# Kernel tuning notes

Hardware: AMD Instinct MI355X
Metric: run time of the kernel (lower is better)

The kernel has to match this reference:

```python
import jax, jax.numpy as jnp
import numpy as np

N = 100000   # nodes
E = 1600000  # edges (avg degree 16)
D = 64       # out_channels (in_channels == out_channels, so no zero-padding step)
L = 2        # GatedGraphConv num_layers


def setup_inputs() -> dict:
    key = jax.random.key(0)
    ks = jax.random.split(key, 11)
    w = lambda k, shape: jax.random.normal(k, shape, jnp.float32) * 0.05
    return {
        "x": jax.random.normal(ks[0], (N, D), jnp.float32),
        "edge_index": jax.random.randint(ks[1], (2, E), 0, N, dtype=jnp.int64),
        "conv_w": w(ks[2], (L, D, D)),        # GatedGraphConv per-layer message weight
        "gru_w_ih": w(ks[3], (3 * D, D)),     # GRUCell input->hidden (r|z|n)
        "gru_w_hh": w(ks[4], (3 * D, D)),     # GRUCell hidden->hidden (r|z|n)
        "gru_b_ih": w(ks[5], (3 * D,)),
        "gru_b_hh": w(ks[6], (3 * D,)),
        "lin_w": w(ks[7], (D, D)),            # nn.Linear(out, out)
        "lin_b": w(ks[8], (D,)),
        "attn_w": w(ks[9], (1, D)),           # nn.Linear(out, 1)
        "attn_b": w(ks[10], (1,)),
    }


def reference(x, edge_index, conv_w, gru_w_ih, gru_w_hh, gru_b_ih, gru_b_hh,
              lin_w, lin_b, attn_w, attn_b):
    src, dst = edge_index[0], edge_index[1]
    h = x  # in_channels == out_channels -> no padding
    for i in range(L):
        m = h @ conv_w[i]  # [N, D] transformed messages
        # gather at source nodes, scatter-add into target nodes
        agg = jax.ops.segment_sum(m[src], dst, num_segments=N)  # [N, D]
        # GRUCell(agg, h)
        gi = agg @ gru_w_ih.T + gru_b_ih  # [N, 3D]
        gh = h @ gru_w_hh.T + gru_b_hh    # [N, 3D]
        i_r, i_z, i_n = jnp.split(gi, 3, axis=1)
        h_r, h_z, h_n = jnp.split(gh, 3, axis=1)
        r = jax.nn.sigmoid(i_r + h_r)
        z = jax.nn.sigmoid(i_z + h_z)
        n = jnp.tanh(i_n + r * h_n)
        h = (1.0 - z) * n + z * h
    y = jax.nn.relu(h) @ lin_w.T + lin_b                 # [N, D]
    attn = jax.nn.softmax(y @ attn_w.T + attn_b, axis=0) # [N, 1], softmax over nodes
    return (attn * y).sum(axis=0, keepdims=True)          # [1, D]
```

## Files before the change

kernel.cpp:

```cpp
#include <hip/hip_runtime.h>


typedef __attribute__((ext_vector_type(8))) short s8v;
typedef __attribute__((ext_vector_type(4))) float f32x4;

#define CSR_CAP 12288

__device__ __forceinline__ unsigned short f32_bf16_rn(float x) {
  unsigned u = __float_as_uint(x);
  u += 0x7FFF + ((u >> 16) & 1);
  return (unsigned short)(u >> 16);
}

__device__ __forceinline__ int wave_incl_scan(int v, int lane) {
#pragma unroll
  for (int d = 1; d < 64; d <<= 1) {
    int u = __shfl_up(v, d);
    if (lane >= d) v += u;
  }
  return v;
}

__device__ __forceinline__ int detect_is64(const int* ei, int E) {
  int nz = 0;
  int lim = (E < 512) ? E : 512;
  for (int i = threadIdx.x; i < lim; i += blockDim.x)
    nz |= (ei[2 * i + 1] != 0);
  return __syncthreads_or(nz) ? 0 : 1;
}

__device__ __forceinline__ void load_edge(const int* ei, int E, int is64,
                                          int e, int& s, int& d) {
  if (is64) { s = ei[2 * e]; d = ei[2 * (E + e)]; }
  else      { s = ei[e];     d = ei[E + e]; }
}

__global__ __launch_bounds__(256) void count_kernel(
    const int* __restrict__ ei, int E,
    int* __restrict__ G, int P, int perBlk, int NB) {
  __shared__ int hist[512];
  int tid = threadIdx.x, b = blockIdx.x;
  for (int i = tid; i < 512; i += 256) hist[i] = 0;
  int is64 = detect_is64(ei, E);
  __syncthreads();
  int e0 = b * perBlk, e1 = min(e0 + perBlk, E);
  for (int e = e0 + tid; e < e1; e += 256) {
    int s, d; load_edge(ei, E, is64, e, s, d);
    atomicAdd(&hist[d >> 8], 1);
  }
  __syncthreads();
  for (int i = tid; i < P; i += 256) G[i * NB + b] = hist[i];
}

__global__ __launch_bounds__(256) void scan2a(int* __restrict__ G,
                                              int* __restrict__ total, int NB) {
  __shared__ int wsum[4];
  int p = blockIdx.x, tid = threadIdx.x, lane = tid & 63, wv = tid >> 6;
  int v = G[p * NB + tid];
  int incl = wave_incl_scan(v, lane);
  if (lane == 63) wsum[wv] = incl;
  __syncthreads();
  if (tid == 0) {
    int a = wsum[0], b2 = wsum[1], c = wsum[2], d = wsum[3];
    total[p] = a + b2 + c + d;
    wsum[0] = 0; wsum[1] = a; wsum[2] = a + b2; wsum[3] = a + b2 + c;
  }
  __syncthreads();
  G[p * NB + tid] = incl - v + wsum[wv];
}

__global__ void scan2b(const int* __restrict__ total, int* __restrict__ partStart,
                       int P) {
  int lane = threadIdx.x;
  int running = 0;
  for (int base = 0; base < P; base += 64) {
    int idx = base + lane;
    int v = (idx < P) ? total[idx] : 0;
    int incl = wave_incl_scan(v, lane);
    int tot = __shfl(incl, 63);
    if (idx < P) partStart[idx] = running + incl - v;
    running += tot;
  }
  if (lane == 0) partStart[P] = running;
}

__global__ __launch_bounds__(256) void scatter_kernel(
    const int* __restrict__ ei, int E,
    const int* __restrict__ G, const int* __restrict__ partStart,
    int* __restrict__ bucket, int P, int perBlk, int NB) {
  __shared__ int cur[512];
  int tid = threadIdx.x, b = blockIdx.x;
  int is64 = detect_is64(ei, E);
  for (int i = tid; i < P; i += 256) cur[i] = partStart[i] + G[i * NB + b];
  __syncthreads();
  int e0 = b * perBlk, e1 = min(e0 + perBlk, E);
  for (int e = e0 + tid; e < e1; e += 256) {
    int s, d; load_edge(ei, E, is64, e, s, d);
    int pos = atomicAdd(&cur[d >> 8], 1);
    bucket[pos] = ((d & 255) << 17) | s;
  }
}

__global__ __launch_bounds__(256) void buildcsr_kernel(
    const int* __restrict__ partStart, const int* __restrict__ bucket,
    int* __restrict__ row_ptr, int* __restrict__ col, int N) {
  __shared__ int stage[CSR_CAP];
  __shared__ int hist[256];
  __shared__ int cur[256];
  __shared__ int wsum[4];
  int p = blockIdx.x, tid = threadIdx.x;
  int beg = partStart[p], end = partStart[p + 1];
  int cnt = end - beg;
  int base = p << 8;
  hist[tid] = 0;
  __syncthreads();
  bool staged = (cnt <= CSR_CAP);
  if (staged) {
    for (int i = tid; i < cnt; i += 256) {
      int v = bucket[beg + i];
      stage[i] = v;
      atomicAdd(&hist[(v >> 17) & 255], 1);
    }
  } else {
    for (int i = tid; i < cnt; i += 256)
      atomicAdd(&hist[(bucket[beg + i] >> 17) & 255], 1);
  }
  __syncthreads();
  int lane = tid & 63, wv = tid >> 6;
  int v = hist[tid];
  int incl = wave_incl_scan(v, lane);
  if (lane == 63) wsum[wv] = incl;
  __syncthreads();
  if (tid == 0) {
    int s0 = wsum[0], s1 = wsum[1], s2 = wsum[2];
    wsum[0] = 0; wsum[1] = s0; wsum[2] = s0 + s1; wsum[3] = s0 + s1 + s2;
  }
  __syncthreads();
  int excl = incl - v + wsum[wv];
  cur[tid] = beg + excl;
  if (base + tid < N) {
    if (tid == 0) row_ptr[base] = beg;
    row_ptr[base + tid + 1] = beg + excl + v;
  }
  __syncthreads();
  if (staged) {
    for (int i = tid; i < cnt; i += 256) {
      int v2 = stage[i];
      int pos = atomicAdd(&cur[(v2 >> 17) & 255], 1);
      col[pos] = v2 & 0x1FFFF;
    }
  } else {
    for (int i = tid; i < cnt; i += 256) {
      int v2 = bucket[beg + i];
      int pos = atomicAdd(&cur[(v2 >> 17) & 255], 1);
      col[pos] = v2 & 0x1FFFF;
    }
  }
}

__global__ void wprep_kernel(const float* __restrict__ conv_w,
                             const float* __restrict__ w_ih,
                             const float* __restrict__ whh,
                             const float* __restrict__ lin_w,
                             unsigned short* __restrict__ Bt,
                             unsigned short* __restrict__ Lt) {
  int idx = blockIdx.x * blockDim.x + threadIdx.x;
  if (idx < 65536) {
    int l = idx >> 15;
    int rr = idx & 32767;
    int c = rr >> 7, p = rr & 127;
    int g = c >> 6, ch = c & 63;
    float val = 0.f;
    if (p < 64) {
      int j = (g == 0) ? ch : (g == 1) ? 64 + ch : (g == 2) ? 128 + ch : -1;
      if (j >= 0) {
        const float* C = conv_w + l * 4096 + p * 64;
        const float* W = w_ih + j * 64;
#pragma unroll 8
        for (int k = 0; k < 64; k++) val += C[k] * W[k];
      }
    } else {
      int q = p - 64;
      if (g == 0)      val = whh[ch * 64 + q];
      else if (g == 1) val = whh[(64 + ch) * 64 + q];
      else if (g == 3) val = whh[(128 + ch) * 64 + q];
    }
    unsigned short hi = f32_bf16_rn(val);
    float fh = __uint_as_float((unsigned)hi << 16);
    unsigned short lo = f32_bf16_rn(val - fh);
    size_t base = (size_t)l * 65536;
    Bt[base + (size_t)c * 128 + p] = hi;
    Bt[base + 32768 + (size_t)c * 128 + p] = lo;
  } else if (idx < 65536 + 4096) {
    int i2 = idx - 65536;
    float val = lin_w[i2];
    unsigned short hi = f32_bf16_rn(val);
    float fh = __uint_as_float((unsigned)hi << 16);
    unsigned short lo = f32_bf16_rn(val - fh);
    Lt[i2] = hi;
    Lt[4096 + i2] = lo;
  }
}

__global__ __launch_bounds__(256) void cvt16_kernel(
    const float* __restrict__ in, unsigned short* __restrict__ out, int n8) {
  int idx = blockIdx.x * blockDim.x + threadIdx.x;
  if (idx >= n8) return;
  const float4* p = (const float4*)(in + (size_t)idx * 8);
  float4 v0 = p[0], v1 = p[1];
  uint4 o;
  o.x = (unsigned)f32_bf16_rn(v0.x) | ((unsigned)f32_bf16_rn(v0.y) << 16);
  o.y = (unsigned)f32_bf16_rn(v0.z) | ((unsigned)f32_bf16_rn(v0.w) << 16);
  o.z = (unsigned)f32_bf16_rn(v1.x) | ((unsigned)f32_bf16_rn(v1.y) << 16);
  o.w = (unsigned)f32_bf16_rn(v1.z) | ((unsigned)f32_bf16_rn(v1.w) << 16);
  *(uint4*)(out + (size_t)idx * 8) = o;
}

__global__ __launch_bounds__(256) void gather_kernel(
    const unsigned short* __restrict__ hb, const int* __restrict__ row_ptr,
    const int* __restrict__ col, float* __restrict__ sout, int N) {
  int gt = blockIdx.x * blockDim.x + threadIdx.x;
  int n = gt >> 6, lane = gt & 63;
  if (n >= N) return;
  int grp = lane >> 4, q = lane & 15;
  int beg = row_ptr[n], end = row_ptr[n + 1];
  float4 a0 = make_float4(0.f, 0.f, 0.f, 0.f);
  float4 a1 = make_float4(0.f, 0.f, 0.f, 0.f);
  int e = beg + grp;
  for (; e + 4 < end; e += 8) {
    int s0 = col[e], s1 = col[e + 4];
    uint2 r0 = *(const uint2*)(hb + (size_t)s0 * 64 + q * 4);
    uint2 r1 = *(const uint2*)(hb + (size_t)s1 * 64 + q * 4);
    a0.x += __uint_as_float(r0.x << 16);
    a0.y += __uint_as_float(r0.x & 0xFFFF0000u);
    a0.z += __uint_as_float(r0.y << 16);
    a0.w += __uint_as_float(r0.y & 0xFFFF0000u);
    a1.x += __uint_as_float(r1.x << 16);
    a1.y += __uint_as_float(r1.x & 0xFFFF0000u);
    a1.z += __uint_as_float(r1.y << 16);
    a1.w += __uint_as_float(r1.y & 0xFFFF0000u);
  }
  if (e < end) {
    int s0 = col[e];
    uint2 r0 = *(const uint2*)(hb + (size_t)s0 * 64 + q * 4);
    a0.x += __uint_as_float(r0.x << 16);
    a0.y += __uint_as_float(r0.x & 0xFFFF0000u);
    a0.z += __uint_as_float(r0.y << 16);
    a0.w += __uint_as_float(r0.y & 0xFFFF0000u);
  }
  a0.x += a1.x; a0.y += a1.y; a0.z += a1.z; a0.w += a1.w;
#pragma unroll
  for (int off = 16; off <= 32; off <<= 1) {
    a0.x += __shfl_xor(a0.x, off);
    a0.y += __shfl_xor(a0.y, off);
    a0.z += __shfl_xor(a0.z, off);
    a0.w += __shfl_xor(a0.w, off);
  }
  if (grp == 0) *(float4*)(sout + (size_t)n * 64 + q * 4) = a0;
}

__global__ __launch_bounds__(256, 2) void gemm_gru_kernel(
    const float* __restrict__ sb, const float* __restrict__ hin,
    float* __restrict__ hout, unsigned short* __restrict__ hb16,
    const unsigned short* __restrict__ bt,
    const float* __restrict__ b_ih, const float* __restrict__ b_hh,
    int N, int ntiles, int wb16) {
  __shared__ short Alds[2 * 64 * 136];
  const int tid = threadIdx.x;
  const int lane = tid & 63, w = tid >> 6;
  const int l15 = lane & 15, ko = (lane >> 4) * 8;

  s8v Bh[4][4], Bl[4][4];
  {
    const int col = 16 * w + l15;
#pragma unroll
    for (int c = 0; c < 4; c++)
#pragma unroll
      for (int kk = 0; kk < 4; kk++) {
        size_t o = (size_t)(64 * c + col) * 128 + kk * 32 + ko;
        Bh[c][kk] = *(const s8v*)(bt + o);
        Bl[c][kk] = *(const s8v*)(bt + 32768 + o);
      }
  }
  const int ch = 16 * w + l15;
  const float br = b_ih[ch] + b_hh[ch];
  const float bz = b_ih[64 + ch] + b_hh[64 + ch];
  const float bin_ = b_ih[128 + ch];
  const float bhn = b_hh[128 + ch];
  const int q4 = (lane >> 4) * 4;
  const int sr = tid >> 2, part = tid & 3;

  for (int tile = blockIdx.x; tile < ntiles; tile += gridDim.x) {
    const int nb = tile * 64;
    {
      int node = nb + sr;
      f32x4 v[8];
      if (node < N) {
        const float* base = (part < 2) ? (sb + (size_t)node * 64 + part * 32)
                                       : (hin + (size_t)node * 64 + (part - 2) * 32);
#pragma unroll
        for (int i = 0; i < 8; i++) v[i] = *(const f32x4*)(base + 4 * i);
      } else {
#pragma unroll
        for (int i = 0; i < 8; i++) v[i] = (f32x4)(0.f);
      }
      short* ah = &Alds[sr * 136 + part * 32];
#pragma unroll
      for (int i2 = 0; i2 < 4; i2++) {
        s8v hv, lv;
#pragma unroll
        for (int e = 0; e < 8; e++) {
          float x = v[i2 * 2 + (e >> 2)][e & 3];
          unsigned short hb = f32_bf16_rn(x);
          float fh = __uint_as_float((unsigned)hb << 16);
          unsigned short lb = f32_bf16_rn(x - fh);
          hv[e] = (short)hb;
          lv[e] = (short)lb;
        }
        *(s8v*)(ah + i2 * 8) = hv;
        *(s8v*)(ah + 64 * 136 + i2 * 8) = lv;
      }
    }
    __syncthreads();

    f32x4 acc[4][4];
#pragma unroll
    for (int m = 0; m < 4; m++)
#pragma unroll
      for (int c = 0; c < 4; c++) acc[m][c] = (f32x4)(0.f);

#pragma unroll
    for (int m = 0; m < 4; m++) {
      const short* arow = &Alds[(16 * m + l15) * 136 + ko];
#pragma unroll
      for (int kk = 0; kk < 4; kk++) {
        s8v a_h = *(const s8v*)(arow + kk * 32);
        s8v a_l = *(const s8v*)(arow + 64 * 136 + kk * 32);
#pragma unroll
        for (int c = 0; c < 4; c++) {
          acc[m][c] = __builtin_amdgcn_mfma_f32_16x16x32_bf16(a_h, Bh[c][kk], acc[m][c], 0, 0, 0);
          acc[m][c] = __builtin_amdgcn_mfma_f32_16x16x32_bf16(a_h, Bl[c][kk], acc[m][c], 0, 0, 0);
          acc[m][c] = __builtin_amdgcn_mfma_f32_16x16x32_bf16(a_l, Bh[c][kk], acc[m][c], 0, 0, 0);
        }
      }
    }

#pragma unroll
    for (int m = 0; m < 4; m++) {
#pragma unroll
      for (int g = 0; g < 4; g++) {
        int loc = 16 * m + q4 + g;
        int node = nb + loc;
        if (node < N) {
          unsigned hi = (unsigned short)Alds[loc * 136 + 64 + ch];
          unsigned lo = (unsigned short)Alds[64 * 136 + loc * 136 + 64 + ch];
          float hold = __uint_as_float(hi << 16) + __uint_as_float(lo << 16);
          float rr = 1.f / (1.f + __expf(-(acc[m][0][g] + br)));
          float zz = 1.f / (1.f + __expf(-(acc[m][1][g] + bz)));
          float narg = acc[m][2][g] + bin_ + rr * (acc[m][3][g] + bhn);
          narg = fminf(fmaxf(narg, -15.f), 15.f);
          float t = __expf(2.f * narg);
          float nn = (t - 1.f) / (t + 1.f);
          float hv = (1.f - zz) * nn + zz * hold;
          hout[(size_t)node * 64 + ch] = hv;
          if (wb16) hb16[(size_t)node * 64 + ch] = f32_bf16_rn(hv);
        }
      }
    }
    __syncthreads();
  }
}

__global__ __launch_bounds__(256, 2) void final_mfma(
    const float* __restrict__ h, const unsigned short* __restrict__ Lt,
    const float* __restrict__ lin_b, const float* __restrict__ attn_w,
    const float* __restrict__ attn_b, float* __restrict__ partials,
    int N, int ntiles) {
  __shared__ short Alds[2 * 64 * 72];
  __shared__ float red[4][64];
  __shared__ float pl[64];
  const int tid = threadIdx.x;
  const int lane = tid & 63, w = tid >> 6;
  const int l15 = lane & 15, ko = (lane >> 4) * 8;
  const int q = lane >> 4;

  s8v Lh[2], Ll[2];
  const int col = 16 * w + l15;
#pragma unroll
  for (int kk = 0; kk < 2; kk++) {
    Lh[kk] = *(const s8v*)(Lt + (size_t)col * 64 + kk * 32 + ko);
    Ll[kk] = *(const s8v*)(Lt + 4096 + (size_t)col * 64 + kk * 32 + ko);
  }
  const float lb = lin_b[col];
  const float aw = attn_w[col];
  const float ab = attn_b[0];
  const int sr = tid >> 2, part = tid & 3;

  float accS = 0.f;
  float accY = 0.f;

  for (int tile = blockIdx.x; tile < ntiles; tile += gridDim.x) {
    const int nb = tile * 64;
    {
      int node = nb + sr;
      f32x4 v[4];
      if (node < N) {
#pragma unroll
        for (int i = 0; i < 4; i++)
          v[i] = *(const f32x4*)(h + (size_t)node * 64 + part * 16 + 4 * i);
      } else {
#pragma unroll
        for (int i = 0; i < 4; i++) v[i] = (f32x4)(0.f);
      }
      short* ah = &Alds[sr * 72 + part * 16];
#pragma unroll
      for (int i2 = 0; i2 < 2; i2++) {
        s8v hv, lv;
#pragma unroll
        for (int e = 0; e < 8; e++) {
          float x = fmaxf(v[i2 * 2 + (e >> 2)][e & 3], 0.f);
          unsigned short hb = f32_bf16_rn(x);
          float fh = __uint_as_float((unsigned)hb << 16);
          unsigned short lo2 = f32_bf16_rn(x - fh);
          hv[e] = (short)hb;
          lv[e] = (short)lo2;
        }
        *(s8v*)(ah + i2 * 8) = hv;
        *(s8v*)(ah + 64 * 72 + i2 * 8) = lv;
      }
    }
    __syncthreads();

    f32x4 acc[4];
#pragma unroll
    for (int m = 0; m < 4; m++) acc[m] = (f32x4)(0.f);
#pragma unroll
    for (int m = 0; m < 4; m++) {
      const short* arow = &Alds[(16 * m + l15) * 72 + ko];
#pragma unroll
      for (int kk = 0; kk < 2; kk++) {
        s8v a_h = *(const s8v*)(arow + kk * 32);
        s8v a_l = *(const s8v*)(arow + 64 * 72 + kk * 32);
        acc[m] = __builtin_amdgcn_mfma_f32_16x16x32_bf16(a_h, Lh[kk], acc[m], 0, 0, 0);
        acc[m] = __builtin_amdgcn_mfma_f32_16x16x32_bf16(a_h, Ll[kk], acc[m], 0, 0, 0);
        acc[m] = __builtin_amdgcn_mfma_f32_16x16x32_bf16(a_l, Lh[kk], acc[m], 0, 0, 0);
      }
    }
    __syncthreads();

    float cc[4][4];
#pragma unroll
    for (int m = 0; m < 4; m++)
#pragma unroll
      for (int g = 0; g < 4; g++) cc[m][g] = (acc[m][g] + lb) * aw;
#pragma unroll
    for (int off = 1; off <= 8; off <<= 1)
#pragma unroll
      for (int m = 0; m < 4; m++)
#pragma unroll
        for (int g = 0; g < 4; g++) cc[m][g] += __shfl_xor(cc[m][g], off);
    if (l15 == 0) {
#pragma unroll
      for (int m = 0; m < 4; m++)
#pragma unroll
        for (int g = 0; g < 4; g++) red[w][16 * m + 4 * q + g] = cc[m][g];
    }
    __syncthreads();
    if (tid < 64) {
      float t = red[0][tid] + red[1][tid] + red[2][tid] + red[3][tid] + ab;
      float p = (nb + tid < N) ? __expf(t) : 0.f;
      pl[tid] = p;
      accS += p;
    }
    __syncthreads();
#pragma unroll
    for (int m = 0; m < 4; m++)
#pragma unroll
      for (int g = 0; g < 4; g++)
        accY += pl[16 * m + 4 * q + g] * (acc[m][g] + lb);
  }

  accY += __shfl_xor(accY, 16);
  accY += __shfl_xor(accY, 32);
  if (lane < 16) partials[(size_t)blockIdx.x * 66 + 16 * w + lane] = accY;
  if (w == 0) {
    float s = accS;
#pragma unroll
    for (int off = 1; off < 64; off <<= 1) s += __shfl_xor(s, off);
    if (lane == 0) partials[(size_t)blockIdx.x * 66 + 64] = s;
  }
}

__global__ void final_p2(const float* __restrict__ partials,
                         float* __restrict__ out, int nb) {
  __shared__ float red[16][65];
  int tid = threadIdx.x;
  int j = tid & 63, grp = tid >> 6;
  float sy = 0.f, ss = 0.f;
  for (int b = grp; b < nb; b += 16) {
    sy += partials[b * 66 + j];
    if (j == 0) ss += partials[b * 66 + 64];
  }
  red[grp][j] = sy;
  if (j == 0) red[grp][64] = ss;
  __syncthreads();
  if (tid < 64) {
    float Y = 0.f, S = 0.f;
#pragma unroll
    for (int i = 0; i < 16; i++) { Y += red[i][tid]; S += red[i][64]; }
    out[tid] = Y / S;
  }
}

extern "C" void kernel_launch(void* const* d_in, const int* in_sizes, int n_in,
                              void* d_out, int out_size, void* d_ws, size_t ws_size,
                              hipStream_t stream) {
  const float* x       = (const float*)d_in[0];
  const int*   ei      = (const int*)d_in[1];
  const float* conv_w  = (const float*)d_in[2];
  const float* gw_ih   = (const float*)d_in[3];
  const float* gw_hh   = (const float*)d_in[4];
  const float* gb_ih   = (const float*)d_in[5];
  const float* gb_hh   = (const float*)d_in[6];
  const float* lin_w   = (const float*)d_in[7];
  const float* lin_b   = (const float*)d_in[8];
  const float* attn_w  = (const float*)d_in[9];
  const float* attn_b  = (const float*)d_in[10];
  float* out = (float*)d_out;

  const int N = in_sizes[0] / 64;
  const int E = in_sizes[1] / 2;
  const int P  = (N + 255) >> 8;
  const int NB = 256;
  const int perBlk = (E + NB - 1) / NB;

  char* ws = (char*)d_ws;
  size_t off = 0;
  auto alloc = [&](size_t bytes) {
    void* p = ws + off;
    off = (off + bytes + 255) & ~(size_t)255;
    return p;
  };
  int*   G         = (int*)alloc((size_t)P * NB * 4);
  int*   total     = (int*)alloc((size_t)P * 4);
  int*   partStart = (int*)alloc((size_t)(P + 1) * 4);
  int*   bucket    = (int*)alloc((size_t)E * 4);
  int*   row_ptr   = (int*)alloc((size_t)(N + 1) * 4);
  int*   colb      = (int*)alloc((size_t)E * 4);
  unsigned short* Bt = (unsigned short*)alloc(2 * 2 * 256 * 128 * 2);
  unsigned short* Lt = (unsigned short*)alloc(2 * 4096 * 2);
  unsigned short* b16 = (unsigned short*)alloc((size_t)N * 64 * 2);
  float* sbuf      = (float*)alloc((size_t)N * 64 * 4);
  float* hbuf      = (float*)alloc((size_t)N * 64 * 4);
  float* partials  = (float*)alloc(1024 * 66 * 4);
  if (off > ws_size) return;

  count_kernel<<<NB, 256, 0, stream>>>(ei, E, G, P, perBlk, NB);
  scan2a<<<P, 256, 0, stream>>>(G, total, NB);
  scan2b<<<1, 64, 0, stream>>>(total, partStart, P);
  scatter_kernel<<<NB, 256, 0, stream>>>(ei, E, G, partStart, bucket, P, perBlk, NB);
  buildcsr_kernel<<<P, 256, 0, stream>>>(partStart, bucket, row_ptr, colb, N);
  wprep_kernel<<<(65536 + 4096 + 255) / 256, 256, 0, stream>>>(conv_w, gw_ih, gw_hh,
                                                               lin_w, Bt, Lt);
  int n8 = (N * 64) / 8;
  cvt16_kernel<<<(n8 + 255) / 256, 256, 0, stream>>>(x, b16, n8);

  int gb = (N * 64 + 255) / 256;
  int ntiles = (N + 63) / 64;
  gather_kernel<<<gb, 256, 0, stream>>>(b16, row_ptr, colb, sbuf, N);
  gemm_gru_kernel<<<512, 256, 0, stream>>>(sbuf, x, hbuf, b16, Bt, gb_ih, gb_hh,
                                           N, ntiles, 1);
  gather_kernel<<<gb, 256, 0, stream>>>(b16, row_ptr, colb, sbuf, N);
  gemm_gru_kernel<<<512, 256, 0, stream>>>(sbuf, hbuf, hbuf, b16, Bt + 65536,
                                           gb_ih, gb_hh, N, ntiles, 0);
  final_mfma<<<512, 256, 0, stream>>>(hbuf, Lt, lin_b, attn_w, attn_b, partials, N, ntiles);
  final_p2<<<1, 1024, 0, stream>>>(partials, out, 512);
}
```

Baseline: 246.7 us.

## Double-buffer LDS tiles in GEMM-GRU kernel to prefetch next tile during MFMA

Restructures the persistent gemm_gru_kernel loop so the global loads for the next 64-node tile are issued before the MFMA work on the current tile. The loaded values are converted to bf16 hi/lo and stored into a second LDS buffer after the GRU epilogue. The aim is to hide global-load latency behind compute. In exchange, LDS doubles to dynamic shared memory, and 32 extra VGPRs stay live across the MFMA section, which could reduce occupancy or cause spills.

```diff
diff --git a/kernel.cpp b/kernel.cpp
--- a/kernel.cpp
+++ b/kernel.cpp
@@ -5,6 +5,9 @@
 typedef __attribute__((ext_vector_type(4))) float f32x4;
 
 #define CSR_CAP 12288
+#define HSTR 136
+#define PLANE (64 * HSTR)
+#define ABUF (2 * PLANE)
 
 __device__ __forceinline__ unsigned short f32_bf16_rn(float x) {
   unsigned u = __float_as_uint(x);
@@ -265,7 +268,7 @@
     const unsigned short* __restrict__ bt,
     const float* __restrict__ b_ih, const float* __restrict__ b_hh,
     int N, int ntiles, int wb16) {
-  __shared__ short Alds[2 * 64 * 136];
+  extern __shared__ short Alds[];
   const int tid = threadIdx.x;
   const int lane = tid & 63, w = tid >> 6;
   const int l15 = lane & 15, ko = (lane >> 4) * 8;
@@ -289,39 +292,52 @@
   const float bhn = b_hh[128 + ch];
   const int q4 = (lane >> 4) * 4;
   const int sr = tid >> 2, part = tid & 3;
-
-  for (int tile = blockIdx.x; tile < ntiles; tile += gridDim.x) {
-    const int nb = tile * 64;
-    {
-      int node = nb + sr;
-      f32x4 v[8];
-      if (node < N) {
-        const float* base = (part < 2) ? (sb + (size_t)node * 64 + part * 32)
-                                       : (hin + (size_t)node * 64 + (part - 2) * 32);
-#pragma unroll
-        for (int i = 0; i < 8; i++) v[i] = *(const f32x4*)(base + 4 * i);
-      } else {
-#pragma unroll
-        for (int i = 0; i < 8; i++) v[i] = (f32x4)(0.f);
-      }
-      short* ah = &Alds[sr * 136 + part * 32];
-#pragma unroll
-      for (int i2 = 0; i2 < 4; i2++) {
-        s8v hv, lv;
-#pragma unroll
-        for (int e = 0; e < 8; e++) {
-          float x = v[i2 * 2 + (e >> 2)][e & 3];
-          unsigned short hb = f32_bf16_rn(x);
-          float fh = __uint_as_float((unsigned)hb << 16);
-          unsigned short lb = f32_bf16_rn(x - fh);
-          hv[e] = (short)hb;
-          lv[e] = (short)lb;
-        }
-        *(s8v*)(ah + i2 * 8) = hv;
-        *(s8v*)(ah + 64 * 136 + i2 * 8) = lv;
-      }
-    }
-    __syncthreads();
+  const int stride = gridDim.x;
+
+  f32x4 v[8];
+  auto issue_loads = [&](int tile) {
+    int node = tile * 64 + sr;
+    if (node < N) {
+      const float* base = (part < 2) ? (sb + (size_t)node * 64 + part * 32)
+                                     : (hin + (size_t)node * 64 + (part - 2) * 32);
+#pragma unroll
+      for (int i = 0; i < 8; i++) v[i] = *(const f32x4*)(base + 4 * i);
+    } else {
+#pragma unroll
+      for (int i = 0; i < 8; i++) v[i] = (f32x4)(0.f);
+    }
+  };
+  auto cvt_store = [&](int buf) {
+    short* ah = &Alds[buf * ABUF + sr * HSTR + part * 32];
+#pragma unroll
+    for (int i2 = 0; i2 < 4; i2++) {
+      s8v hv, lv;
+#pragma unroll
+      for (int e = 0; e < 8; e++) {
+        float x = v[i2 * 2 + (e >> 2)][e & 3];
+        unsigned short hb = f32_bf16_rn(x);
+        float fh = __uint_as_float((unsigned)hb << 16);
+        unsigned short lb = f32_bf16_rn(x - fh);
+        hv[e] = (short)hb;
+        lv[e] = (short)lb;
+      }
+      *(s8v*)(ah + i2 * 8) = hv;
+      *(s8v*)(ah + PLANE + i2 * 8) = lv;
+    }
+  };
+
+  const int tile0 = blockIdx.x;
+  if (tile0 < ntiles) {
+    issue_loads(tile0);
+    cvt_store(0);
+  }
+  __syncthreads();
+  int cur = 0;
+
+  for (int tile = tile0; tile < ntiles; tile += stride) {
+    const int nxt = tile + stride;
+    const bool has_nxt = (nxt < ntiles);
+    if (has_nxt) issue_loads(nxt);
 
     f32x4 acc[4][4];
 #pragma unroll
@@ -329,13 +345,14 @@
 #pragma unroll
       for (int c = 0; c < 4; c++) acc[m][c] = (f32x4)(0.f);
 
+    const short* abase = &Alds[cur * ABUF];
 #pragma unroll
     for (int m = 0; m < 4; m++) {
-      const short* arow = &Alds[(16 * m + l15) * 136 + ko];
+      const short* arow = abase + (16 * m + l15) * HSTR + ko;
 #pragma unroll
       for (int kk = 0; kk < 4; kk++) {
         s8v a_h = *(const s8v*)(arow + kk * 32);
-        s8v a_l = *(const s8v*)(arow + 64 * 136 + kk * 32);
+        s8v a_l = *(const s8v*)(arow + PLANE + kk * 32);
 #pragma unroll
         for (int c = 0; c < 4; c++) {
           acc[m][c] = __builtin_amdgcn_mfma_f32_16x16x32_bf16(a_h, Bh[c][kk], acc[m][c], 0, 0, 0);
@@ -345,6 +362,7 @@
       }
     }
 
+    const int nb = tile * 64;
 #pragma unroll
     for (int m = 0; m < 4; m++) {
 #pragma unroll
@@ -352,8 +370,8 @@
         int loc = 16 * m + q4 + g;
         int node = nb + loc;
         if (node < N) {
-          unsigned hi = (unsigned short)Alds[loc * 136 + 64 + ch];
-          unsigned lo = (unsigned short)Alds[64 * 136 + loc * 136 + 64 + ch];
+          unsigned hi = (unsigned short)abase[loc * HSTR + 64 + ch];
+          unsigned lo = (unsigned short)abase[PLANE + loc * HSTR + 64 + ch];
           float hold = __uint_as_float(hi << 16) + __uint_as_float(lo << 16);
           float rr = 1.f / (1.f + __expf(-(acc[m][0][g] + br)));
           float zz = 1.f / (1.f + __expf(-(acc[m][1][g] + bz)));
@@ -367,7 +385,10 @@
         }
       }
     }
+
+    if (has_nxt) cvt_store(cur ^ 1);
     __syncthreads();
+    cur ^= 1;
   }
 }
 
@@ -565,14 +586,19 @@
   int n8 = (N * 64) / 8;
   cvt16_kernel<<<(n8 + 255) / 256, 256, 0, stream>>>(x, b16, n8);
 
+  size_t gemm_lds = (size_t)2 * ABUF * sizeof(short);
+  hipFuncSetAttribute((const void*)gemm_gru_kernel,
+                      hipFuncAttributeMaxDynamicSharedMemorySize, (int)gemm_lds);
+
   int gb = (N * 64 + 255) / 256;
   int ntiles = (N + 63) / 64;
   gather_kernel<<<gb, 256, 0, stream>>>(b16, row_ptr, colb, sbuf, N);
-  gemm_gru_kernel<<<512, 256, 0, stream>>>(sbuf, x, hbuf, b16, Bt, gb_ih, gb_hh,
-                                           N, ntiles, 1);
+  gemm_gru_kernel<<<512, 256, gemm_lds, stream>>>(sbuf, x, hbuf, b16, Bt,
+                                                  gb_ih, gb_hh, N, ntiles, 1);
   gather_kernel<<<gb, 256, 0, stream>>>(b16, row_ptr, colb, sbuf, N);
-  gemm_gru_kernel<<<512, 256, 0, stream>>>(sbuf, hbuf, hbuf, b16, Bt + 65536,
-                                           gb_ih, gb_hh, N, ntiles, 0);
+  gemm_gru_kernel<<<512, 256, gemm_lds, stream>>>(sbuf, hbuf, hbuf, b16,
+                                                  Bt + 65536, gb_ih, gb_hh,
+                                                  N, ntiles, 0);
   final_mfma<<<512, 256, 0, stream>>>(hbuf, Lt, lin_b, attn_w, attn_b, partials, N, ntiles);
   final_p2<<<1, 1024, 0, stream>>>(partials, out, 512);
 }
```

New measurement: 259.1 us. +5.0%, slower.

## Fuse neighbor gather into GRU GEMM kernel and drop low-half of aggregated input

Applied to the files above, without the earlier changes.

Removes the separate gather kernel and the fp32 aggregate buffer: each GEMM tile now gathers its 64 nodes' neighbor rows from the bf16 feature array directly into shared memory. The aggregated part is stored only as a single bf16 value, so the error-compensation MFMA pass on that half of K is dropped, cutting MFMA work. Separate bf16 buffers for x and h avoid a read/write race in layer 2. The cost is that the irregular gather now runs inside a 2-blocks-per-CU, 512-block kernel with one thread per quarter-row, which may hide memory latency less well, and rounding the aggregate to bf16 reduces accuracy.

```diff
diff --git a/kernel.cpp b/kernel.cpp
--- a/kernel.cpp
+++ b/kernel.cpp
@@ -5,6 +5,8 @@
 typedef __attribute__((ext_vector_type(4))) float f32x4;
 
 #define CSR_CAP 12288
+#define HSTR 136
+#define LSTR 72
 
 __device__ __forceinline__ unsigned short f32_bf16_rn(float x) {
   unsigned u = __float_as_uint(x);
@@ -216,68 +218,38 @@
   *(uint4*)(out + (size_t)idx * 8) = o;
 }
 
-__global__ __launch_bounds__(256) void gather_kernel(
-    const unsigned short* __restrict__ hb, const int* __restrict__ row_ptr,
-    const int* __restrict__ col, float* __restrict__ sout, int N) {
-  int gt = blockIdx.x * blockDim.x + threadIdx.x;
-  int n = gt >> 6, lane = gt & 63;
-  if (n >= N) return;
-  int grp = lane >> 4, q = lane & 15;
-  int beg = row_ptr[n], end = row_ptr[n + 1];
-  float4 a0 = make_float4(0.f, 0.f, 0.f, 0.f);
-  float4 a1 = make_float4(0.f, 0.f, 0.f, 0.f);
-  int e = beg + grp;
-  for (; e + 4 < end; e += 8) {
-    int s0 = col[e], s1 = col[e + 4];
-    uint2 r0 = *(const uint2*)(hb + (size_t)s0 * 64 + q * 4);
-    uint2 r1 = *(const uint2*)(hb + (size_t)s1 * 64 + q * 4);
-    a0.x += __uint_as_float(r0.x << 16);
-    a0.y += __uint_as_float(r0.x & 0xFFFF0000u);
-    a0.z += __uint_as_float(r0.y << 16);
-    a0.w += __uint_as_float(r0.y & 0xFFFF0000u);
-    a1.x += __uint_as_float(r1.x << 16);
-    a1.y += __uint_as_float(r1.x & 0xFFFF0000u);
-    a1.z += __uint_as_float(r1.y << 16);
-    a1.w += __uint_as_float(r1.y & 0xFFFF0000u);
-  }
-  if (e < end) {
-    int s0 = col[e];
-    uint2 r0 = *(const uint2*)(hb + (size_t)s0 * 64 + q * 4);
-    a0.x += __uint_as_float(r0.x << 16);
-    a0.y += __uint_as_float(r0.x & 0xFFFF0000u);
-    a0.z += __uint_as_float(r0.y << 16);
-    a0.w += __uint_as_float(r0.y & 0xFFFF0000u);
-  }
-  a0.x += a1.x; a0.y += a1.y; a0.z += a1.z; a0.w += a1.w;
-#pragma unroll
-  for (int off = 16; off <= 32; off <<= 1) {
-    a0.x += __shfl_xor(a0.x, off);
-    a0.y += __shfl_xor(a0.y, off);
-    a0.z += __shfl_xor(a0.z, off);
-    a0.w += __shfl_xor(a0.w, off);
-  }
-  if (grp == 0) *(float4*)(sout + (size_t)n * 64 + q * 4) = a0;
+__device__ __forceinline__ void acc_u4(const uint4& r, float* a) {
+  a[0] += __uint_as_float(r.x << 16);
+  a[1] += __uint_as_float(r.x & 0xFFFF0000u);
+  a[2] += __uint_as_float(r.y << 16);
+  a[3] += __uint_as_float(r.y & 0xFFFF0000u);
+  a[4] += __uint_as_float(r.z << 16);
+  a[5] += __uint_as_float(r.z & 0xFFFF0000u);
+  a[6] += __uint_as_float(r.w << 16);
+  a[7] += __uint_as_float(r.w & 0xFFFF0000u);
 }
 
 __global__ __launch_bounds__(256, 2) void gemm_gru_kernel(
-    const float* __restrict__ sb, const float* __restrict__ hin,
+    const unsigned short* __restrict__ src16, const int* __restrict__ row_ptr,
+    const int* __restrict__ col, const float* __restrict__ hin,
     float* __restrict__ hout, unsigned short* __restrict__ hb16,
     const unsigned short* __restrict__ bt,
     const float* __restrict__ b_ih, const float* __restrict__ b_hh,
     int N, int ntiles, int wb16) {
-  __shared__ short Alds[2 * 64 * 136];
+  __shared__ short Ahi[64 * HSTR];
+  __shared__ short Alo[64 * LSTR];
   const int tid = threadIdx.x;
   const int lane = tid & 63, w = tid >> 6;
   const int l15 = lane & 15, ko = (lane >> 4) * 8;
 
   s8v Bh[4][4], Bl[4][4];
   {
-    const int col = 16 * w + l15;
+    const int colc = 16 * w + l15;
 #pragma unroll
     for (int c = 0; c < 4; c++)
 #pragma unroll
       for (int kk = 0; kk < 4; kk++) {
-        size_t o = (size_t)(64 * c + col) * 128 + kk * 32 + ko;
+        size_t o = (size_t)(64 * c + colc) * 128 + kk * 32 + ko;
         Bh[c][kk] = *(const s8v*)(bt + o);
         Bl[c][kk] = *(const s8v*)(bt + 32768 + o);
       }
@@ -288,38 +260,73 @@
   const float bin_ = b_ih[128 + ch];
   const float bhn = b_hh[128 + ch];
   const int q4 = (lane >> 4) * 4;
-  const int sr = tid >> 2, part = tid & 3;
+  const int g = tid >> 2, qc = tid & 3;
 
   for (int tile = blockIdx.x; tile < ntiles; tile += gridDim.x) {
     const int nb = tile * 64;
+    const int node = nb + g;
     {
-      int node = nb + sr;
-      f32x4 v[8];
+      float a[16];
+#pragma unroll
+      for (int i = 0; i < 16; i++) a[i] = 0.f;
       if (node < N) {
-        const float* base = (part < 2) ? (sb + (size_t)node * 64 + part * 32)
-                                       : (hin + (size_t)node * 64 + (part - 2) * 32);
-#pragma unroll
-        for (int i = 0; i < 8; i++) v[i] = *(const f32x4*)(base + 4 * i);
+        int beg = row_ptr[node], end = row_ptr[node + 1];
+        int e = beg;
+        for (; e + 2 <= end; e += 2) {
+          const unsigned short* b0 = src16 + (size_t)col[e] * 64 + qc * 16;
+          const unsigned short* b1 = src16 + (size_t)col[e + 1] * 64 + qc * 16;
+          uint4 r0 = *(const uint4*)b0;
+          uint4 r1 = *(const uint4*)(b0 + 8);
+          uint4 r2 = *(const uint4*)b1;
+          uint4 r3 = *(const uint4*)(b1 + 8);
+          acc_u4(r0, a); acc_u4(r1, a + 8);
+          acc_u4(r2, a); acc_u4(r3, a + 8);
+        }
+        if (e < end) {
+          const unsigned short* b0 = src16 + (size_t)col[e] * 64 + qc * 16;
+          uint4 r0 = *(const uint4*)b0;
+          uint4 r1 = *(const uint4*)(b0 + 8);
+          acc_u4(r0, a); acc_u4(r1, a + 8);
+        }
+      }
+      s8v sv0, sv1;
+#pragma unroll
+      for (int i = 0; i < 8; i++) {
+        sv0[i] = (short)f32_bf16_rn(a[i]);
+        sv1[i] = (short)f32_bf16_rn(a[8 + i]);
+      }
+      short* sh = &Ahi[g * HSTR + qc * 16];
+      *(s8v*)sh = sv0;
+      *(s8v*)(sh + 8) = sv1;
+    }
+    {
+      f32x4 v[4];
+      if (node < N) {
+#pragma unroll
+        for (int i = 0; i < 4; i++)
+          v[i] = *(const f32x4*)(hin + (size_t)node * 64 + qc * 16 + 4 * i);
       } else {
 #pragma unroll
-        for (int i = 0; i < 8; i++) v[i] = (f32x4)(0.f);
-      }
-      short* ah = &Alds[sr * 136 + part * 32];
-#pragma unroll
-      for (int i2 = 0; i2 < 4; i2++) {
-        s8v hv, lv;
-#pragma unroll
-        for (int e = 0; e < 8; e++) {
-          float x = v[i2 * 2 + (e >> 2)][e & 3];
-          unsigned short hb = f32_bf16_rn(x);
-          float fh = __uint_as_float((unsigned)hb << 16);
-          unsigned short lb = f32_bf16_rn(x - fh);
-          hv[e] = (short)hb;
-          lv[e] = (short)lb;
-        }
-        *(s8v*)(ah + i2 * 8) = hv;
-        *(s8v*)(ah + 64 * 136 + i2 * 8) = lv;
-      }
+        for (int i = 0; i < 4; i++) v[i] = (f32x4)(0.f);
+      }
+      s8v hv0, hv1, lv0, lv1;
+#pragma unroll
+      for (int i = 0; i < 8; i++) {
+        float x0 = v[i >> 2][i & 3];
+        float x1 = v[2 + (i >> 2)][i & 3];
+        unsigned short hb0 = f32_bf16_rn(x0);
+        unsigned short hb1 = f32_bf16_rn(x1);
+        hv0[i] = (short)hb0;
+        hv1[i] = (short)hb1;
+        lv0[i] = (short)f32_bf16_rn(x0 - __uint_as_float((unsigned)hb0 << 16));
+        lv1[i] = (short)f32_bf16_rn(x1 - __uint_as_float((unsigned)hb1 << 16));
+      }
+      short* hh = &Ahi[g * HSTR + 64 + qc * 16];
+      *(s8v*)hh = hv0;
+      *(s8v*)(hh + 8) = hv1;
+      short* hl = &Alo[g * LSTR + qc * 16];
+      *(s8v*)hl = lv0;
+      *(s8v*)(hl + 8) = lv1;
     }
     __syncthreads();
 
@@ -331,39 +338,44 @@
 
 #pragma unroll
     for (int m = 0; m < 4; m++) {
-      const short* arow = &Alds[(16 * m + l15) * 136 + ko];
+      const short* arh = &Ahi[(16 * m + l15) * HSTR + ko];
+      const short* arl = &Alo[(16 * m + l15) * LSTR + ko];
 #pragma unroll
       for (int kk = 0; kk < 4; kk++) {
-        s8v a_h = *(const s8v*)(arow + kk * 32);
-        s8v a_l = *(const s8v*)(arow + 64 * 136 + kk * 32);
+        s8v a_h = *(const s8v*)(arh + kk * 32);
 #pragma unroll
         for (int c = 0; c < 4; c++) {
           acc[m][c] = __builtin_amdgcn_mfma_f32_16x16x32_bf16(a_h, Bh[c][kk], acc[m][c], 0, 0, 0);
           acc[m][c] = __builtin_amdgcn_mfma_f32_16x16x32_bf16(a_h, Bl[c][kk], acc[m][c], 0, 0, 0);
-          acc[m][c] = __builtin_amdgcn_mfma_f32_16x16x32_bf16(a_l, Bh[c][kk], acc[m][c], 0, 0, 0);
         }
+        if (kk >= 2) {
+          s8v a_l = *(const s8v*)(arl + (kk - 2) * 32);
+#pragma unroll
+          for (int c = 0; c < 4; c++)
+            acc[m][c] = __builtin_amdgcn_mfma_f32_16x16x32_bf16(a_l, Bh[c][kk], acc[m][c], 0, 0, 0);
+        }
       }
     }
 
 #pragma unroll
     for (int m = 0; m < 4; m++) {
 #pragma unroll
-      for (int g = 0; g < 4; g++) {
-        int loc = 16 * m + q4 + g;
-        int node = nb + loc;
-        if (node < N) {
-          unsigned hi = (unsigned short)Alds[loc * 136 + 64 + ch];
-          unsigned lo = (unsigned short)Alds[64 * 136 + loc * 136 + 64 + ch];
+      for (int gg = 0; gg < 4; gg++) {
+        int loc = 16 * m + q4 + gg;
+        int nd = nb + loc;
+        if (nd < N) {
+          unsigned hi = (unsigned short)Ahi[loc * HSTR + 64 + ch];
+          unsigned lo = (unsigned short)Alo[loc * LSTR + ch];
           float hold = __uint_as_float(hi << 16) + __uint_as_float(lo << 16);
-          float rr = 1.f / (1.f + __expf(-(acc[m][0][g] + br)));
-          float zz = 1.f / (1.f + __expf(-(acc[m][1][g] + bz)));
-          float narg = acc[m][2][g] + bin_ + rr * (acc[m][3][g] + bhn);
+          float rr = 1.f / (1.f + __expf(-(acc[m][0][gg] + br)));
+          float zz = 1.f / (1.f + __expf(-(acc[m][1][gg] + bz)));
+          float narg = acc[m][2][gg] + bin_ + rr * (acc[m][3][gg] + bhn);
           narg = fminf(fmaxf(narg, -15.f), 15.f);
           float t = __expf(2.f * narg);
           float nn = (t - 1.f) / (t + 1.f);
           float hv = (1.f - zz) * nn + zz * hold;
-          hout[(size_t)node * 64 + ch] = hv;
-          if (wb16) hb16[(size_t)node * 64 + ch] = f32_bf16_rn(hv);
+          hout[(size_t)nd * 64 + ch] = hv;
+          if (wb16) hb16[(size_t)nd * 64 + ch] = f32_bf16_rn(hv);
         }
       }
     }
@@ -547,10 +559,10 @@
   int*   bucket    = (int*)alloc((size_t)E * 4);
   int*   row_ptr   = (int*)alloc((size_t)(N + 1) * 4);
   int*   colb      = (int*)alloc((size_t)E * 4);
-  unsigned short* Bt = (unsigned short*)alloc(2 * 2 * 256 * 128 * 2);
-  unsigned short* Lt = (unsigned short*)alloc(2 * 4096 * 2);
-  unsigned short* b16 = (unsigned short*)alloc((size_t)N * 64 * 2);
-  float* sbuf      = (float*)alloc((size_t)N * 64 * 4);
+  unsigned short* Bt  = (unsigned short*)alloc(2 * 2 * 256 * 128 * 2);
+  unsigned short* Lt  = (unsigned short*)alloc(2 * 4096 * 2);
+  unsigned short* b16x = (unsigned short*)alloc((size_t)N * 64 * 2);
+  unsigned short* b16h = (unsigned short*)alloc((size_t)N * 64 * 2);
   float* hbuf      = (float*)alloc((size_t)N * 64 * 4);
   float* partials  = (float*)alloc(1024 * 66 * 4);
   if (off > ws_size) return;
@@ -563,16 +575,13 @@
   wprep_kernel<<<(65536 + 4096 + 255) / 256, 256, 0, stream>>>(conv_w, gw_ih, gw_hh,
                                                                lin_w, Bt, Lt);
   int n8 = (N * 64) / 8;
-  cvt16_kernel<<<(n8 + 255) / 256, 256, 0, stream>>>(x, b16, n8);
-
-  int gb = (N * 64 + 255) / 256;
+  cvt16_kernel<<<(n8 + 255) / 256, 256, 0, stream>>>(x, b16x, n8);
+
   int ntiles = (N + 63) / 64;
-  gather_kernel<<<gb, 256, 0, stream>>>(b16, row_ptr, colb, sbuf, N);
-  gemm_gru_kernel<<<512, 256, 0, stream>>>(sbuf, x, hbuf, b16, Bt, gb_ih, gb_hh,
-                                           N, ntiles, 1);
-  gather_kernel<<<gb, 256, 0, stream>>>(b16, row_ptr, colb, sbuf, N);
-  gemm_gru_kernel<<<512, 256, 0, stream>>>(sbuf, hbuf, hbuf, b16, Bt + 65536,
-                                           gb_ih, gb_hh, N, ntiles, 0);
+  gemm_gru_kernel<<<512, 256, 0, stream>>>(b16x, row_ptr, colb, x, hbuf, b16h,
+                                           Bt, gb_ih, gb_hh, N, ntiles, 1);
+  gemm_gru_kernel<<<512, 256, 0, stream>>>(b16h, row_ptr, colb, hbuf, hbuf, b16h,
+                                           Bt + 65536, gb_ih, gb_hh, N, ntiles, 0);
   final_mfma<<<512, 256, 0, stream>>>(hbuf, Lt, lin_b, attn_w, attn_b, partials, N, ntiles);
   final_p2<<<1, 1024, 0, stream>>>(partials, out, 512);
 }
```

After: 235.0 us. -4.8%, faster.
